# Kernel optimization log

Measured on AMD Instinct MI355X. Metric: run time of the kernel, lower is better.

## Reference

```python
import jax, jax.numpy as jnp
import numpy as np

HEAD_NUM = 16
HEAD_SIZE = 64
D_MODEL = 1024
B, N = 8, 1024
MASK_PENALTY = 1e8


def setup_inputs() -> dict:
    key = jax.random.key(0)
    k1, k2, k3 = jax.random.split(key, 3)
    inputs = jax.random.normal(k1, (B, N, D_MODEL), dtype=jnp.float32)
    mask = jax.random.randint(k2, (B, N), 0, 2).astype(jnp.float32)
    # glorot-uniform-ish init for kernel [H, 3, d_model, head_size]
    limit = float(np.sqrt(6.0 / (D_MODEL + HEAD_SIZE)))
    kernel = jax.random.uniform(k3, (HEAD_NUM, 3, D_MODEL, HEAD_SIZE),
                                dtype=jnp.float32, minval=-limit, maxval=limit)
    return {"inputs": inputs, "mask": mask, "kernel": kernel}


def reference(inputs, mask, kernel):
    # inputs: [B,N,d], kernel: [H,3,d,s]
    q = jnp.einsum('bnd,hds->bhns', inputs, kernel[:, 0])
    k = jnp.einsum('bnd,hds->bhns', inputs, kernel[:, 1])
    v = jnp.einsum('bnd,hds->bhns', inputs, kernel[:, 2])
    # NOTE: original never applies 1/sqrt(head_size) scaling (faithful).
    scores = jnp.einsum('bhns,bhms->bhnm', q, k)  # [B,H,N,N]
    # additive mask: outer product of padding mask, penalty on masked pairs
    pair_mask = mask[:, None, :, None] * mask[:, None, None, :]  # [B,1,N,N]
    scores = scores - MASK_PENALTY * (1.0 - pair_mask)
    attn = jax.nn.softmax(scores, axis=-1)
    out = jnp.einsum('bhnm,bhms->bhns', attn, v)  # [B,H,N,s]
    # original permutes to [B,N,s,H] then flattens -> head axis fastest
    out = jnp.transpose(out, (0, 2, 3, 1))  # [B,N,s,H]
    return out.reshape(out.shape[0], out.shape[1], HEAD_SIZE * HEAD_NUM)
```

## Files before the change

kernel.cpp:

```cpp
#include <hip/hip_runtime.h>
#include <math.h>

#define BB 8
#define NN 1024
#define DD 1024
#define HH 16
#define SS 64
#define BH (BB*HH)

typedef _Float16 half8 __attribute__((ext_vector_type(8)));
typedef _Float16 half4v __attribute__((ext_vector_type(4)));
typedef float floatx4 __attribute__((ext_vector_type(4)));

#define MFMA16(A, B, C) __builtin_amdgcn_mfma_f32_16x16x32_f16((A), (B), (C), 0, 0, 0)

__device__ __forceinline__ void gload16(const _Float16* g, _Float16* l) {
    __builtin_amdgcn_global_load_lds(
        (const __attribute__((address_space(1))) void*)g,
        (__attribute__((address_space(3))) void*)l,
        16, 0, 0);
}

__global__ __launch_bounds__(256) void split_x(
    const float* __restrict__ X, _Float16* __restrict__ Xh, _Float16* __restrict__ Xl)
{
    int idx = (blockIdx.x * 256 + threadIdx.x) * 4;
    float4 x4 = *(const float4*)(X + idx);
    float xs[4] = {x4.x, x4.y, x4.z, x4.w};
    half4v h, l;
    #pragma unroll
    for (int i = 0; i < 4; i++) {
        _Float16 hi = (_Float16)xs[i];
        h[i] = hi;
        l[i] = (_Float16)(xs[i] - (float)hi);
    }
    *(half4v*)(Xh + idx) = h;
    *(half4v*)(Xl + idx) = l;
}

__global__ __launch_bounds__(256) void split_wt(
    const float* __restrict__ W, _Float16* __restrict__ Wth, _Float16* __restrict__ Wtl)
{
    __shared__ float tile[64][68];
    const int hc = blockIdx.x, d0 = blockIdx.y * 64;
    const int t = threadIdx.x;
    {
        int i = t >> 2, sq = (t & 3) * 16;
        const float* src = W + ((size_t)hc * DD + d0 + i) * SS + sq;
        #pragma unroll
        for (int u = 0; u < 4; u++) {
            float4 v = *(const float4*)(src + 4 * u);
            tile[i][sq + 4 * u + 0] = v.x; tile[i][sq + 4 * u + 1] = v.y;
            tile[i][sq + 4 * u + 2] = v.z; tile[i][sq + 4 * u + 3] = v.w;
        }
    }
    __syncthreads();
    {
        int s = t >> 2, jq = (t & 3) * 16;
        _Float16 hbuf[16], lbuf[16];
        #pragma unroll
        for (int u = 0; u < 16; u++) {
            float x = tile[jq + u][s];
            _Float16 hi = (_Float16)x;
            hbuf[u] = hi;
            lbuf[u] = (_Float16)(x - (float)hi);
        }
        size_t off = (size_t)hc * SS * DD + (size_t)s * DD + d0 + jq;
        *(half8*)(Wth + off)     = *(half8*)(hbuf);
        *(half8*)(Wth + off + 8) = *(half8*)(hbuf + 8);
        *(half8*)(Wtl + off)     = *(half8*)(lbuf);
        *(half8*)(Wtl + off + 8) = *(half8*)(lbuf + 8);
    }
}

__global__ __launch_bounds__(256, 2) void qkv_mfma(
    const _Float16* __restrict__ Xh, const _Float16* __restrict__ Xl,
    const _Float16* __restrict__ Wth, const _Float16* __restrict__ Wtl,
    _Float16* __restrict__ Qh, _Float16* __restrict__ Ql,
    _Float16* __restrict__ Kh, _Float16* __restrict__ Kl,
    _Float16* __restrict__ Vt)
{
    const int flat = blockIdx.y * 64 + blockIdx.x;
    const int swz  = (flat & 7) * 192 + (flat >> 3);
    const int bx = swz & 63;
    const int by = swz >> 6;
    const int hc0 = by * 2;
    const int r0  = bx * 128;

    const int tid = threadIdx.x;
    const int wave = tid >> 6, lane = tid & 63;
    const int l16 = lane & 15, quad = lane >> 4;
    const int wr = wave >> 1, wc = wave & 1;

    __shared__ _Float16 sAh[128 * 32];
    __shared__ _Float16 sAl[128 * 32];
    __shared__ _Float16 sBh[128 * 32];
    __shared__ _Float16 sBl[128 * 32];

    floatx4 acc[4][4];
    #pragma unroll
    for (int i = 0; i < 4; i++)
        #pragma unroll
        for (int j = 0; j < 4; j++) acc[i][j] = (floatx4){0.f, 0.f, 0.f, 0.f};

    const _Float16* Ab_h = Xh  + (size_t)r0 * DD;
    const _Float16* Ab_l = Xl  + (size_t)r0 * DD;
    const _Float16* Bb_h = Wth + (size_t)hc0 * SS * DD;
    const _Float16* Bb_l = Wtl + (size_t)hc0 * SS * DD;

    for (int k0 = 0; k0 < DD; k0 += 32) {
        #pragma unroll
        for (int i = 0; i < 2; i++) {
            const int g = tid + 256 * i;
            const int row = g >> 2, kc = (g & 3) * 8;
            const size_t go = (size_t)row * DD + k0 + kc;
            gload16(Ab_h + go, &sAh[g * 8]);
            gload16(Ab_l + go, &sAl[g * 8]);
            gload16(Bb_h + go, &sBh[g * 8]);
            gload16(Bb_l + go, &sBl[g * 8]);
        }
        __syncthreads();

        half8 Ah[4], Al[4], Bh[4], Bl[4];
        #pragma unroll
        for (int t = 0; t < 4; t++) {
            const int ar = wr * 64 + 16 * t + l16;
            const int br = wc * 64 + 16 * t + l16;
            Ah[t] = *(const half8*)&sAh[ar * 32 + quad * 8];
            Al[t] = *(const half8*)&sAl[ar * 32 + quad * 8];
            Bh[t] = *(const half8*)&sBh[br * 32 + quad * 8];
            Bl[t] = *(const half8*)&sBl[br * 32 + quad * 8];
        }
        #pragma unroll
        for (int i = 0; i < 4; i++)
            #pragma unroll
            for (int j = 0; j < 4; j++)
                acc[i][j] = MFMA16(Ah[i], Bh[j], acc[i][j]);
        #pragma unroll
        for (int i = 0; i < 4; i++)
            #pragma unroll
            for (int j = 0; j < 4; j++)
                acc[i][j] = MFMA16(Ah[i], Bl[j], acc[i][j]);
        #pragma unroll
        for (int i = 0; i < 4; i++)
            #pragma unroll
            for (int j = 0; j < 4; j++)
                acc[i][j] = MFMA16(Al[i], Bh[j], acc[i][j]);
        __syncthreads();
    }

    const int hc = hc0 + wc;
    const int h = hc / 3, c = hc % 3;
    const int rowbase = r0 + wr * 64;
    if (c == 2) {
        #pragma unroll
        for (int i = 0; i < 4; i++)
            #pragma unroll
            for (int j = 0; j < 4; j++) {
                int tok0 = rowbase + 16 * i + 4 * quad;
                int b = tok0 >> 10, n0 = tok0 & 1023;
                half4v pk;
                #pragma unroll
                for (int r = 0; r < 4; r++) pk[r] = (_Float16)acc[i][j][r];
                *(half4v*)(Vt + ((size_t)(b * HH + h) * SS + 16 * j + l16) * NN + n0) = pk;
            }
    } else {
        _Float16* Ph = (c == 0) ? Qh : Kh;
        _Float16* Pl = (c == 0) ? Ql : Kl;
        #pragma unroll
        for (int i = 0; i < 4; i++)
            #pragma unroll
            for (int j = 0; j < 4; j++)
                #pragma unroll
                for (int r = 0; r < 4; r++) {
                    int tok = rowbase + 16 * i + 4 * quad + r;
                    int b = tok >> 10, n = tok & 1023;
                    float v = acc[i][j][r];
                    _Float16 vh = (_Float16)v;
                    _Float16 vl = (_Float16)(v - (float)vh);
                    size_t off = ((size_t)(b * HH + h) * NN + n) * SS + 16 * j + l16;
                    Ph[off] = vh; Pl[off] = vl;
                }
    }
}

__global__ __launch_bounds__(256) void attn_mfma(
    const _Float16* __restrict__ Qh, const _Float16* __restrict__ Ql,
    const _Float16* __restrict__ Kh, const _Float16* __restrict__ Kl,
    const _Float16* __restrict__ Vt,
    const float* __restrict__ mask,
    float* __restrict__ out)
{
    const int bh = blockIdx.x, qt = blockIdx.y;
    const int b = bh >> 4, h = bh & 15;
    const int tid = threadIdx.x;
    const int wave = tid >> 6, lane = tid & 63;
    const int l16 = lane & 15, quad = lane >> 4;

    __shared__ float Ms[NN];
    __shared__ _Float16 KhS[2][64 * 64];
    __shared__ _Float16 KlS[2][64 * 64];
    __shared__ _Float16 VS [2][64 * 64];
    __shared__ _Float16 Plds[4][32][72];

    *(float4*)&Ms[tid * 4] = *(const float4*)(mask + b * NN + tid * 4);

    half8 G[6];
    auto stage_load = [&](int kt_) {
        #pragma unroll
        for (int i = 0; i < 2; i++) {
            int g = tid + 256 * i;
            int row = g >> 3;
            int c = (g & 7) ^ (row & 7);
            size_t ko = ((size_t)bh * NN + kt_ * 64 + row) * SS + c * 8;
            G[i]     = *(const half8*)(Kh + ko);
            G[2 + i] = *(const half8*)(Kl + ko);
            G[4 + i] = *(const half8*)(Vt + ((size_t)bh * SS + row) * NN
                                       + (size_t)kt_ * 64 + c * 8);
        }
    };
    auto stage_store = [&](int buf) {
        #pragma unroll
        for (int i = 0; i < 2; i++) {
            int g = tid + 256 * i;
            *(half8*)&KhS[buf][g * 8] = G[i];
            *(half8*)&KlS[buf][g * 8] = G[2 + i];
            *(half8*)&VS [buf][g * 8] = G[4 + i];
        }
    };

    stage_load(0);
    stage_store(0);
    __syncthreads();

    const int qrow0 = qt * 128 + wave * 32;
    half8 Aqh[2][2], Aql[2][2];
    #pragma unroll
    for (int g = 0; g < 2; g++) {
        const size_t qbase = ((size_t)bh * NN + qrow0 + 16 * g + l16) * SS + quad * 8;
        Aqh[g][0] = *(const half8*)(Qh + qbase);
        Aqh[g][1] = *(const half8*)(Qh + qbase + 32);
        Aql[g][0] = *(const half8*)(Ql + qbase);
        Aql[g][1] = *(const half8*)(Ql + qbase + 32);
    }

    float qm[2][4], m_old[2][4], l_sum[2][4];
    floatx4 accO[2][4];
    #pragma unroll
    for (int g = 0; g < 2; g++) {
        #pragma unroll
        for (int r = 0; r < 4; r++) {
            qm[g][r] = Ms[qrow0 + 16 * g + quad * 4 + r];
            m_old[g][r] = -3.0e38f;
            l_sum[g][r] = 0.f;
        }
        #pragma unroll
        for (int j = 0; j < 4; j++) accO[g][j] = (floatx4){0.f, 0.f, 0.f, 0.f};
    }

    const int sw = l16 & 7;

    for (int kt = 0; kt < 16; kt++) {
        const int cur = kt & 1;
        if (kt < 15) stage_load(kt + 1);

        floatx4 accS[2][4];
        #pragma unroll
        for (int g = 0; g < 2; g++)
            #pragma unroll
            for (int jt = 0; jt < 4; jt++) accS[g][jt] = (floatx4){0.f, 0.f, 0.f, 0.f};
        #pragma unroll
        for (int jt = 0; jt < 4; jt++) {
            const int rowK = jt * 16 + l16;
            const _Float16* krh = &KhS[cur][rowK * 64];
            const _Float16* krl = &KlS[cur][rowK * 64];
            half8 Bh0 = *(const half8*)&krh[((quad    ) ^ sw) * 8];
            half8 Bh1 = *(const half8*)&krh[((quad + 4) ^ sw) * 8];
            half8 Bl0 = *(const half8*)&krl[((quad    ) ^ sw) * 8];
            half8 Bl1 = *(const half8*)&krl[((quad + 4) ^ sw) * 8];
            #pragma unroll
            for (int g = 0; g < 2; g++) {
                accS[g][jt] = MFMA16(Aqh[g][0], Bh0, accS[g][jt]);
                accS[g][jt] = MFMA16(Aqh[g][1], Bh1, accS[g][jt]);
                accS[g][jt] = MFMA16(Aqh[g][0], Bl0, accS[g][jt]);
                accS[g][jt] = MFMA16(Aqh[g][1], Bl1, accS[g][jt]);
                accS[g][jt] = MFMA16(Aql[g][0], Bh0, accS[g][jt]);
                accS[g][jt] = MFMA16(Aql[g][1], Bh1, accS[g][jt]);
            }
        }
        float km[4];
        #pragma unroll
        for (int jt = 0; jt < 4; jt++) km[jt] = Ms[kt * 64 + jt * 16 + l16];
        #pragma unroll
        for (int g = 0; g < 2; g++)
            #pragma unroll
            for (int jt = 0; jt < 4; jt++)
                #pragma unroll
                for (int r = 0; r < 4; r++)
                    accS[g][jt][r] -= 1.0e8f * (1.0f - qm[g][r] * km[jt]);

        #pragma unroll
        for (int g = 0; g < 2; g++) {
            float alpha[4];
            #pragma unroll
            for (int r = 0; r < 4; r++) {
                float mt = fmaxf(fmaxf(accS[g][0][r], accS[g][1][r]),
                                 fmaxf(accS[g][2][r], accS[g][3][r]));
                #pragma unroll
                for (int off = 1; off < 16; off <<= 1)
                    mt = fmaxf(mt, __shfl_xor(mt, off, 64));
                float mn = fmaxf(m_old[g][r], mt);
                alpha[r] = __expf(m_old[g][r] - mn);
                m_old[g][r] = mn;
                float ls = 0.f;
                #pragma unroll
                for (int jt = 0; jt < 4; jt++) {
                    float pj = __expf(accS[g][jt][r] - mn);
                    accS[g][jt][r] = pj;
                    ls += pj;
                }
                #pragma unroll
                for (int off = 1; off < 16; off <<= 1)
                    ls += __shfl_xor(ls, off, 64);
                l_sum[g][r] = l_sum[g][r] * alpha[r] + ls;
            }
            #pragma unroll
            for (int j = 0; j < 4; j++)
                #pragma unroll
                for (int r = 0; r < 4; r++)
                    accO[g][j][r] *= alpha[r];

            #pragma unroll
            for (int jt = 0; jt < 4; jt++)
                #pragma unroll
                for (int r = 0; r < 4; r++)
                    Plds[wave][16 * g + quad * 4 + r][((jt ^ quad) << 4) + l16] =
                        (_Float16)accS[g][jt][r];
        }

        #pragma unroll
        for (int ks = 0; ks < 2; ks++) {
            int cbase = (((2 * ks + (quad >> 1)) ^ (l16 >> 2)) << 4) + (quad & 1) * 8;
            half8 Ap[2];
            #pragma unroll
            for (int g = 0; g < 2; g++)
                Ap[g] = *(const half8*)&Plds[wave][16 * g + l16][cbase];
            #pragma unroll
            for (int j = 0; j < 4; j++) {
                half8 Bv = *(const half8*)&VS[cur][(j * 16 + l16) * 64
                                                   + (((ks * 4 + quad) ^ sw) * 8)];
                #pragma unroll
                for (int g = 0; g < 2; g++)
                    accO[g][j] = MFMA16(Ap[g], Bv, accO[g][j]);
            }
        }

        if (kt < 15) {
            stage_store(1 - cur);
            __syncthreads();
        }
    }

    #pragma unroll
    for (int g = 0; g < 2; g++)
        #pragma unroll
        for (int r = 0; r < 4; r++) {
            float inv = 1.f / l_sum[g][r];
            int qrow = qrow0 + 16 * g + quad * 4 + r;
            #pragma unroll
            for (int j = 0; j < 4; j++)
                out[((size_t)(b * NN + qrow)) * (SS * HH) + (j * 16 + l16) * HH + h] =
                    accO[g][j][r] * inv;
        }
}

__global__ __launch_bounds__(256) void qkv_kernel(
    const float* __restrict__ X, const float* __restrict__ W, float* __restrict__ qkv)
{
    const int ttile = blockIdx.x;
    const int hc    = blockIdx.y;
    const int h     = hc / 3, c = hc % 3;
    const int tid = threadIdx.x;
    const int tx = tid & 15, ty = tid >> 4;
    __shared__ float As[32][68];
    __shared__ float Bs[32][68];
    const float* Wb = W + (size_t)hc * DD * SS;
    const int row0 = ttile * 64;
    float acc[4][4];
    #pragma unroll
    for (int i = 0; i < 4; i++)
        #pragma unroll
        for (int j = 0; j < 4; j++) acc[i][j] = 0.f;
    for (int k0 = 0; k0 < DD; k0 += 32) {
        #pragma unroll
        for (int l = 0; l < 2; l++) {
            int i = tid + l * 256;
            int r = i >> 3;
            int kq = (i & 7) * 4;
            float4 x4 = *(const float4*)(X + (size_t)(row0 + r) * DD + k0 + kq);
            As[kq + 0][r] = x4.x; As[kq + 1][r] = x4.y;
            As[kq + 2][r] = x4.z; As[kq + 3][r] = x4.w;
        }
        #pragma unroll
        for (int l = 0; l < 2; l++) {
            int i = tid + l * 256;
            int kr = i >> 4;
            int sq = (i & 15) * 4;
            *(float4*)&Bs[kr][sq] = *(const float4*)(Wb + (size_t)(k0 + kr) * SS + sq);
        }
        __syncthreads();
        #pragma unroll
        for (int kk = 0; kk < 32; kk++) {
            float4 a4 = *(const float4*)&As[kk][ty * 4];
            float4 b4 = *(const float4*)&Bs[kk][tx * 4];
            float a[4] = {a4.x, a4.y, a4.z, a4.w};
            float bb[4] = {b4.x, b4.y, b4.z, b4.w};
            #pragma unroll
            for (int i = 0; i < 4; i++)
                #pragma unroll
                for (int j = 0; j < 4; j++)
                    acc[i][j] = fmaf(a[i], bb[j], acc[i][j]);
        }
        __syncthreads();
    }
    float* outp = qkv + (size_t)c * BH * NN * SS;
    #pragma unroll
    for (int i = 0; i < 4; i++) {
        int tg = row0 + ty * 4 + i;
        int b = tg >> 10, n = tg & 1023;
        float4 v4 = make_float4(acc[i][0], acc[i][1], acc[i][2], acc[i][3]);
        *(float4*)(outp + ((size_t)(b * HH + h) * NN + n) * SS + tx * 4) = v4;
    }
}

__global__ __launch_bounds__(256) void attn_kernel(
    const float* __restrict__ qkv,
    const float* __restrict__ mask,
    float* __restrict__ out)
{
    const int qt = blockIdx.x, h = blockIdx.y, b = blockIdx.z;
    const int tid = threadIdx.x;
    const int tx = tid & 15, ty = tid >> 4;
    const int bh = b * HH + h;
    const float* Q = qkv + (size_t)bh * NN * SS;
    const float* K = qkv + (size_t)BH * NN * SS + (size_t)bh * NN * SS;
    const float* V = qkv + 2 * (size_t)BH * NN * SS + (size_t)bh * NN * SS;

    __shared__ float QsT[64][68];
    __shared__ float KsT[64][68];
    __shared__ float Vs [64][68];
    __shared__ float PsT[64][68];
    __shared__ float Ms[NN];

    {
        float4 mm = *(const float4*)(mask + b * NN + tid * 4);
        *(float4*)&Ms[tid * 4] = mm;
    }
    #pragma unroll
    for (int l = 0; l < 4; l++) {
        int i = tid + l * 256;
        int r = i >> 4, sq = (i & 15) * 4;
        float4 x4 = *(const float4*)(Q + (size_t)(qt * 64 + r) * SS + sq);
        QsT[sq + 0][r] = x4.x; QsT[sq + 1][r] = x4.y;
        QsT[sq + 2][r] = x4.z; QsT[sq + 3][r] = x4.w;
    }
    __syncthreads();

    float m_old[4], l_sum[4], O[4][4], qm[4];
    #pragma unroll
    for (int i = 0; i < 4; i++) {
        qm[i] = Ms[qt * 64 + ty * 4 + i];
        m_old[i] = -3.0e38f; l_sum[i] = 0.f;
        #pragma unroll
        for (int j = 0; j < 4; j++) O[i][j] = 0.f;
    }

    for (int kt = 0; kt < 16; kt++) {
        #pragma unroll
        for (int l = 0; l < 4; l++) {
            int i = tid + l * 256;
            int r = i >> 4, sq = (i & 15) * 4;
            float4 k4 = *(const float4*)(K + (size_t)(kt * 64 + r) * SS + sq);
            KsT[sq + 0][r] = k4.x; KsT[sq + 1][r] = k4.y;
            KsT[sq + 2][r] = k4.z; KsT[sq + 3][r] = k4.w;
            float4 v4 = *(const float4*)(V + (size_t)(kt * 64 + r) * SS + sq);
            *(float4*)&Vs[r][sq] = v4;
        }
        __syncthreads();

        float sc[4][4];
        #pragma unroll
        for (int i = 0; i < 4; i++)
            #pragma unroll
            for (int j = 0; j < 4; j++) sc[i][j] = 0.f;
        #pragma unroll 8
        for (int s = 0; s < 64; s++) {
            float4 a4 = *(const float4*)&QsT[s][ty * 4];
            float4 b4 = *(const float4*)&KsT[s][tx * 4];
            float a[4] = {a4.x, a4.y, a4.z, a4.w};
            float bb[4] = {b4.x, b4.y, b4.z, b4.w};
            #pragma unroll
            for (int i = 0; i < 4; i++)
                #pragma unroll
                for (int j = 0; j < 4; j++)
                    sc[i][j] = fmaf(a[i], bb[j], sc[i][j]);
        }
        float km[4];
        #pragma unroll
        for (int j = 0; j < 4; j++) km[j] = Ms[kt * 64 + tx * 4 + j];
        #pragma unroll
        for (int i = 0; i < 4; i++)
            #pragma unroll
            for (int j = 0; j < 4; j++) {
                float pen = 1.0e8f * (1.0f - qm[i] * km[j]);
                sc[i][j] = sc[i][j] - pen;
            }

        #pragma unroll
        for (int i = 0; i < 4; i++) {
            float mt = fmaxf(fmaxf(sc[i][0], sc[i][1]), fmaxf(sc[i][2], sc[i][3]));
            #pragma unroll
            for (int off = 1; off < 16; off <<= 1)
                mt = fmaxf(mt, __shfl_xor(mt, off, 64));
            float mn = fmaxf(m_old[i], mt);
            float alpha = __expf(m_old[i] - mn);
            float p[4];
            #pragma unroll
            for (int j = 0; j < 4; j++) p[j] = __expf(sc[i][j] - mn);
            float ls = (p[0] + p[1]) + (p[2] + p[3]);
            #pragma unroll
            for (int off = 1; off < 16; off <<= 1)
                ls += __shfl_xor(ls, off, 64);
            l_sum[i] = l_sum[i] * alpha + ls;
            m_old[i] = mn;
            #pragma unroll
            for (int j = 0; j < 4; j++) {
                O[i][j] *= alpha;
                PsT[tx * 4 + j][ty * 4 + i] = p[j];
            }
        }
        __syncthreads();

        #pragma unroll 8
        for (int kj = 0; kj < 64; kj++) {
            float4 p4 = *(const float4*)&PsT[kj][ty * 4];
            float4 v4 = *(const float4*)&Vs[kj][tx * 4];
            float p[4] = {p4.x, p4.y, p4.z, p4.w};
            float vv[4] = {v4.x, v4.y, v4.z, v4.w};
            #pragma unroll
            for (int i = 0; i < 4; i++)
                #pragma unroll
                for (int j = 0; j < 4; j++)
                    O[i][j] = fmaf(p[i], vv[j], O[i][j]);
        }
        __syncthreads();
    }

    #pragma unroll
    for (int i = 0; i < 4; i++) {
        int qrow = qt * 64 + ty * 4 + i;
        float inv = 1.f / l_sum[i];
        #pragma unroll
        for (int j = 0; j < 4; j++) {
            int s = tx * 4 + j;
            out[((size_t)(b * NN + qrow)) * (SS * HH) + s * HH + h] = O[i][j] * inv;
        }
    }
}

extern "C" void kernel_launch(void* const* d_in, const int* in_sizes, int n_in,
                              void* d_out, int out_size, void* d_ws, size_t ws_size,
                              hipStream_t stream) {
    const float* X    = (const float*)d_in[0];
    const float* mask = (const float*)d_in[1];
    const float* W    = (const float*)d_in[2];
    float* out = (float*)d_out;

    const size_t x_elems  = (size_t)BB * NN * DD;
    const size_t w_elems  = (size_t)HH * 3 * SS * DD;
    const size_t qk_elems = (size_t)BH * NN * SS;
    const size_t need_fast = (2 * x_elems + 2 * w_elems + 5 * qk_elems) * sizeof(_Float16);

    if (ws_size >= need_fast) {
        _Float16* Xh  = (_Float16*)d_ws;
        _Float16* Xl  = Xh  + x_elems;
        _Float16* Wth = Xl  + x_elems;
        _Float16* Wtl = Wth + w_elems;
        _Float16* Qh  = Wtl + w_elems;
        _Float16* Ql  = Qh  + qk_elems;
        _Float16* Kh  = Ql  + qk_elems;
        _Float16* Kl  = Kh  + qk_elems;
        _Float16* Vt  = Kl  + qk_elems;

        split_x<<<dim3((unsigned)(x_elems / 1024)), dim3(256), 0, stream>>>(X, Xh, Xl);
        split_wt<<<dim3(48, 16), dim3(256), 0, stream>>>(W, Wth, Wtl);
        qkv_mfma<<<dim3(64, 24), dim3(256), 0, stream>>>(Xh, Xl, Wth, Wtl, Qh, Ql, Kh, Kl, Vt);
        attn_mfma<<<dim3(128, 8), dim3(256), 0, stream>>>(Qh, Ql, Kh, Kl, Vt, mask, out);
    } else if (ws_size >= 3ull * BH * NN * SS * sizeof(float)) {
        float* qkv = (float*)d_ws;
        qkv_kernel<<<dim3(128, 48), dim3(256), 0, stream>>>(X, W, qkv);
        attn_kernel<<<dim3(16, 16, 8), dim3(256), 0, stream>>>(qkv, mask, out);
    }
}
```

Measured before the change: 459.4 us.

## Read K and V straight from global memory instead of double-buffered LDS staging

Drops the shared-memory double buffers for K-high, K-low and V along with the per-tile syncthreads. Each wave now loads its MFMA B operands directly from global memory through the cache, and a launch-bounds occupancy hint of 4 is added. The aim is to cut LDS traffic, barrier stalls and register use so more blocks fit per CU. The cost is that four waves, and every query-tile block, re-read the same K/V tiles from L2, and global load latency is no longer hidden by explicit prefetch.

Result: slower. 660.1 us (+43.7%).

```diff
diff --git a/kernel.cpp b/kernel.cpp
--- a/kernel.cpp
+++ b/kernel.cpp
@@ -184,7 +184,7 @@
     }
 }
 
-__global__ __launch_bounds__(256) void attn_mfma(
+__global__ __launch_bounds__(256, 4) void attn_mfma(
     const _Float16* __restrict__ Qh, const _Float16* __restrict__ Ql,
     const _Float16* __restrict__ Kh, const _Float16* __restrict__ Kl,
     const _Float16* __restrict__ Vt,
@@ -198,40 +198,14 @@
     const int l16 = lane & 15, quad = lane >> 4;
 
     __shared__ float Ms[NN];
-    __shared__ _Float16 KhS[2][64 * 64];
-    __shared__ _Float16 KlS[2][64 * 64];
-    __shared__ _Float16 VS [2][64 * 64];
     __shared__ _Float16 Plds[4][32][72];
 
     *(float4*)&Ms[tid * 4] = *(const float4*)(mask + b * NN + tid * 4);
-
-    half8 G[6];
-    auto stage_load = [&](int kt_) {
-        #pragma unroll
-        for (int i = 0; i < 2; i++) {
-            int g = tid + 256 * i;
-            int row = g >> 3;
-            int c = (g & 7) ^ (row & 7);
-            size_t ko = ((size_t)bh * NN + kt_ * 64 + row) * SS + c * 8;
-            G[i]     = *(const half8*)(Kh + ko);
-            G[2 + i] = *(const half8*)(Kl + ko);
-            G[4 + i] = *(const half8*)(Vt + ((size_t)bh * SS + row) * NN
-                                       + (size_t)kt_ * 64 + c * 8);
-        }
-    };
-    auto stage_store = [&](int buf) {
-        #pragma unroll
-        for (int i = 0; i < 2; i++) {
-            int g = tid + 256 * i;
-            *(half8*)&KhS[buf][g * 8] = G[i];
-            *(half8*)&KlS[buf][g * 8] = G[2 + i];
-            *(half8*)&VS [buf][g * 8] = G[4 + i];
-        }
-    };
-
-    stage_load(0);
-    stage_store(0);
     __syncthreads();
+
+    const _Float16* Kbh = Kh + (size_t)bh * NN * SS;
+    const _Float16* Kbl = Kl + (size_t)bh * NN * SS;
+    const _Float16* Vb  = Vt + (size_t)bh * SS * NN;
 
     const int qrow0 = qt * 128 + wave * 32;
     half8 Aqh[2][2], Aql[2][2];
@@ -258,12 +232,7 @@
         for (int j = 0; j < 4; j++) accO[g][j] = (floatx4){0.f, 0.f, 0.f, 0.f};
     }
 
-    const int sw = l16 & 7;
-
     for (int kt = 0; kt < 16; kt++) {
-        const int cur = kt & 1;
-        if (kt < 15) stage_load(kt + 1);
-
         floatx4 accS[2][4];
         #pragma unroll
         for (int g = 0; g < 2; g++)
@@ -271,13 +240,11 @@
             for (int jt = 0; jt < 4; jt++) accS[g][jt] = (floatx4){0.f, 0.f, 0.f, 0.f};
         #pragma unroll
         for (int jt = 0; jt < 4; jt++) {
-            const int rowK = jt * 16 + l16;
-            const _Float16* krh = &KhS[cur][rowK * 64];
-            const _Float16* krl = &KlS[cur][rowK * 64];
-            half8 Bh0 = *(const half8*)&krh[((quad    ) ^ sw) * 8];
-            half8 Bh1 = *(const half8*)&krh[((quad + 4) ^ sw) * 8];
-            half8 Bl0 = *(const half8*)&krl[((quad    ) ^ sw) * 8];
-            half8 Bl1 = *(const half8*)&krl[((quad + 4) ^ sw) * 8];
+            const size_t krow = (size_t)(kt * 64 + jt * 16 + l16) * SS + quad * 8;
+            half8 Bh0 = *(const half8*)(Kbh + krow);
+            half8 Bh1 = *(const half8*)(Kbh + krow + 32);
+            half8 Bl0 = *(const half8*)(Kbl + krow);
+            half8 Bl1 = *(const half8*)(Kbl + krow + 32);
             #pragma unroll
             for (int g = 0; g < 2; g++) {
                 accS[g][jt] = MFMA16(Aqh[g][0], Bh0, accS[g][jt]);
@@ -347,17 +314,12 @@
                 Ap[g] = *(const half8*)&Plds[wave][16 * g + l16][cbase];
             #pragma unroll
             for (int j = 0; j < 4; j++) {
-                half8 Bv = *(const half8*)&VS[cur][(j * 16 + l16) * 64
-                                                   + (((ks * 4 + quad) ^ sw) * 8)];
+                half8 Bv = *(const half8*)(Vb + (size_t)(j * 16 + l16) * NN
+                                           + kt * 64 + (ks * 4 + quad) * 8);
                 #pragma unroll
                 for (int g = 0; g < 2; g++)
                     accO[g][j] = MFMA16(Ap[g], Bv, accO[g][j]);
             }
-        }
-
-        if (kt < 15) {
-            stage_store(1 - cur);
-            __syncthreads();
         }
     }
 
```
